# Kernel optimization log

Measured on AMD Instinct MI355X. Metric: run time of the kernel, lower is better.

## Reference

```python
import jax, jax.numpy as jnp
import numpy as np

N = 50000       # nodes
E = 800000      # edges (avg degree 16)
IN = 256        # in_features
HEAD = 4        # attention heads (conv1/conv2 out_channels)
F_OUT = 32      # mlp output features per head


def setup_inputs() -> dict:
    key = jax.random.key(0)
    ks = jax.random.split(key, 6)
    feat = jax.random.normal(ks[0], (N, IN), dtype=jnp.float32)
    edge_index = jax.random.randint(ks[1], (2, E), 0, N, dtype=jnp.int64)
    s = 1.0 / np.sqrt(IN)
    # mlp: Linear(IN -> HEAD*F_OUT)
    W_mlp = jax.random.uniform(ks[2], (IN, HEAD * F_OUT), jnp.float32, -s, s)
    b_mlp = jnp.zeros((HEAD * F_OUT,), jnp.float32)
    # conv1/conv2: 1x1 Conv1d(IN -> HEAD) == linear projection
    W1 = jax.random.uniform(ks[3], (HEAD, IN), jnp.float32, -s, s)
    b1 = jnp.zeros((HEAD,), jnp.float32)
    W2 = jax.random.uniform(ks[4], (HEAD, IN), jnp.float32, -s, s)
    b2 = jnp.zeros((HEAD,), jnp.float32)
    eps = jnp.zeros((1,), jnp.float32)  # trainable eps, init 0
    return {"feat": feat, "edge_index": edge_index, "W_mlp": W_mlp,
            "b_mlp": b_mlp, "W1": W1, "b1": b1, "W2": W2, "b2": b2,
            "eps": eps}


def reference(feat, edge_index, W_mlp, b_mlp, W1, b1, W2, b2, eps):
    n = feat.shape[0]
    head = W1.shape[0]
    # mlp: [N, IN] -> [N, head*F] -> [head, N, F]
    x = (feat @ W_mlp + b_mlp).reshape(n, head, -1).transpose(1, 0, 2)
    # 1x1 conv projections -> per-node attention logits [head, N]
    h1 = (feat @ W1.T + b1).T
    h2 = (feat @ W2.T + b2).T
    src = edge_index[0]  # edge[0]
    dst = edge_index[1]  # edge[1]
    # per-edge attention value, relu (dropout=0 -> identity): [head, E]
    v = jax.nn.relu(h1[:, src] + h2[:, dst])
    # gather neighbor features and weight: [head, E, F]
    msg = x[:, dst, :] * v[:, :, None]
    # scatter-add into destination nodes indexed by src: [N, head, F]
    agg = jax.ops.segment_sum(msg.transpose(1, 0, 2), src, num_segments=n)
    h_prime = agg.transpose(1, 0, 2) + eps[0] * x   # [head, N, F]
    # permute(1,0,2).reshape(N, -1) -> [N, head*F]
    return h_prime.transpose(1, 0, 2).reshape(n, -1)
```

## Files before the change

kernel.cpp:

```cpp
#include <hip/hip_runtime.h>

#define NN   50000
#define EE   800000
#define INF  256
#define COUT 128
#define BTROWS 144
#define PROJ_BLOCKS 782
#define CAP  52

#define NB   196
#define BCAP 4608
#define EPB  2048
#define SC_BLOCKS ((EE + EPB - 1) / EPB)
#define BT_BLOCKS 144

typedef __attribute__((ext_vector_type(8))) short short8;
typedef __attribute__((ext_vector_type(4))) float f32x4;

__device__ __forceinline__ float b2f(unsigned short u) {
    union { unsigned int i; float f; } c;
    c.i = ((unsigned int)u) << 16;
    return c.f;
}
__device__ __forceinline__ unsigned short f2b(float f) {
    union { float f; unsigned int i; } c;
    c.f = f;
    unsigned int i = c.i;
    unsigned int lsb = (i >> 16) & 1u;
    i += 0x7fffu + lsb;
    return (unsigned short)(i >> 16);
}
__device__ __forceinline__ float blo(unsigned int u) {
    union { unsigned int i; float f; } c; c.i = u << 16; return c.f;
}
__device__ __forceinline__ float bhi(unsigned int u) {
    union { unsigned int i; float f; } c; c.i = u & 0xffff0000u; return c.f;
}

__global__ __launch_bounds__(256) void bt_scatter_kernel(
    const float* __restrict__ Wm, const float* __restrict__ W1,
    const float* __restrict__ W2,
    unsigned short* __restrict__ BT,
    const int* __restrict__ edge,
    int* __restrict__ bcnt,
    unsigned int* __restrict__ bedges)
{
    __shared__ int lhist[NB];
    __shared__ int lbase[NB];
    const int t = threadIdx.x;

    if (blockIdx.x < BT_BLOCKS) {
        const int n = blockIdx.x;
        const int k = t;
        float v;
        if      (n < 128) v = Wm[k * COUT + n];
        else if (n < 132) v = W1[(n - 128) * INF + k];
        else if (n < 136) v = W2[(n - 132) * INF + k];
        else              v = 0.f;
        BT[n * INF + k] = f2b(v);
        return;
    }

    if (t < NB) lhist[t] = 0;
    __syncthreads();

    const int e0 = (blockIdx.x - BT_BLOCKS) * EPB;
    int s[8], d[8], pos[8];
    #pragma unroll
    for (int k = 0; k < 8; k++) {
        const int e = e0 + k * 256 + t;
        if (e < EE) {
            s[k] = edge[e];
            d[k] = edge[EE + e];
            pos[k] = atomicAdd(&lhist[s[k] >> 8], 1);
        } else {
            pos[k] = -1;
        }
    }
    __syncthreads();
    if (t < NB) lbase[t] = atomicAdd(&bcnt[t * 16], lhist[t]);
    __syncthreads();
    #pragma unroll
    for (int k = 0; k < 8; k++) {
        if (pos[k] >= 0) {
            const int b = s[k] >> 8;
            const int p = lbase[b] + pos[k];
            if (p < BCAP)
                bedges[b * BCAP + p] =
                    ((unsigned int)(s[k] & 255) << 16) | (unsigned int)d[k];
        }
    }
}

#define LSTRIDE 72
#define SMEM_A_BYTES (64 * LSTRIDE * 2)
#define SMEM_BYTES   (SMEM_A_BYTES + BTROWS * LSTRIDE * 2)
__global__ __launch_bounds__(256) void proj_build_kernel(
    const float* __restrict__ feat,
    const unsigned short* __restrict__ BT,
    const float* __restrict__ bm,
    const float* __restrict__ b1,
    const float* __restrict__ b2,
    unsigned short* __restrict__ x_out,
    unsigned short* __restrict__ hh,
    const unsigned int* __restrict__ bedges,
    const int* __restrict__ bcnt,
    unsigned short* __restrict__ sdst,
    int* __restrict__ cursor)
{
    __shared__ alignas(16) char smem[SMEM_BYTES];
    const int t = threadIdx.x;

    if (blockIdx.x >= PROJ_BLOCKS) {
        unsigned short* ladj = (unsigned short*)smem;
        int* lcur = (int*)(smem + 26624);
        const int b = blockIdx.x - PROJ_BLOCKS;
        lcur[t] = 0;
        __syncthreads();

        const int cnt = min(bcnt[b * 16], BCAP);
        for (int i = t; i < cnt; i += 256) {
            const unsigned int pk = bedges[b * BCAP + i];
            const int n = (int)(pk >> 16);
            const int p = atomicAdd(&lcur[n], 1);
            if (p < CAP) ladj[n * CAP + p] = (unsigned short)(pk & 0xffffu);
        }
        __syncthreads();

        const int node0 = b << 8;
        const int nvalid = min(256, NN - node0);
        const int nu8 = nvalid * (CAP / 4);
        unsigned long long* gs = (unsigned long long*)(sdst + (size_t)node0 * CAP);
        const unsigned long long* ls = (const unsigned long long*)ladj;
        for (int i = t; i < nu8; i += 256) gs[i] = ls[i];
        if (t < nvalid) cursor[node0 + t] = min(lcur[t], CAP);
        return;
    }

    short* lA = (short*)smem;
    short* lB = (short*)(smem + SMEM_A_BYTES);

    const int lane  = t & 63;
    const int wave  = t >> 6;
    const int quad  = lane >> 4;
    const int col   = lane & 15;
    const int node0 = blockIdx.x * 64;

    const int arow = t >> 4;
    const int ac4  = t & 15;

    f32x4 acc[9];
    #pragma unroll
    for (int i = 0; i < 9; i++) acc[i] = (f32x4){0.f, 0.f, 0.f, 0.f};

    float4 fr[4][4];
    #pragma unroll
    for (int kc = 0; kc < 4; kc++) {
        #pragma unroll
        for (int p = 0; p < 4; p++) {
            const int grow = node0 + p * 16 + arow;
            fr[kc][p] = (grow < NN)
                ? *(const float4*)(feat + grow * INF + kc * 64 + ac4 * 4)
                : make_float4(0.f, 0.f, 0.f, 0.f);
        }
    }

    #pragma unroll
    for (int kc = 0; kc < 4; kc++) {
        const int k0 = kc * 64;
        #pragma unroll
        for (int p = 0; p < 4; p++) {
            short4 s;
            s.x = (short)f2b(fr[kc][p].x); s.y = (short)f2b(fr[kc][p].y);
            s.z = (short)f2b(fr[kc][p].z); s.w = (short)f2b(fr[kc][p].w);
            *(short4*)&lA[(p * 16 + arow) * LSTRIDE + ac4 * 4] = s;
        }
        #pragma unroll
        for (int p = 0; p < 5; p++) {
            const int idx = p * 256 + t;
            if (idx < (BTROWS * 64) / 8) {
                const int row = idx >> 3;
                const int c8  = idx & 7;
                uint4 u = *(const uint4*)(BT + row * INF + k0 + c8 * 8);
                *(uint4*)&lB[row * LSTRIDE + c8 * 8] = u;
            }
        }
        __syncthreads();

        #pragma unroll
        for (int ks = 0; ks < 2; ks++) {
            short8 a = *(const short8*)&lA[(wave * 16 + col) * LSTRIDE + ks * 32 + quad * 8];
            #pragma unroll
            for (int nt = 0; nt < 9; nt++) {
                short8 b = *(const short8*)&lB[(nt * 16 + col) * LSTRIDE + ks * 32 + quad * 8];
                acc[nt] = __builtin_amdgcn_mfma_f32_16x16x32_bf16(a, b, acc[nt], 0, 0, 0);
            }
        }
        __syncthreads();
    }

    const int rbase = node0 + wave * 16 + quad * 4;
    #pragma unroll
    for (int nt = 0; nt < 8; nt++) {
        const float bias = bm[nt * 16 + col];
        #pragma unroll
        for (int r = 0; r < 4; r++) {
            const int row = rbase + r;
            if (row < NN) x_out[row * COUT + nt * 16 + col] = f2b(acc[nt][r] + bias);
        }
    }
    if (col < 8) {
        const float bias = (col < 4) ? b1[col] : b2[col - 4];
        #pragma unroll
        for (int r = 0; r < 4; r++) {
            const int row = rbase + r;
            if (row < NN) hh[row * 8 + col] = f2b(acc[8][r] + bias);
        }
    }
}

__global__ __launch_bounds__(256) void accum_kernel(
    const int* __restrict__ cursor,
    const unsigned short* __restrict__ sdst,
    const unsigned short* __restrict__ x,
    const unsigned short* __restrict__ hh,
    const float* __restrict__ eps,
    float* __restrict__ out)
{
    const int lane = threadIdx.x & 63;
    const int node = blockIdx.x * 4 + (threadIdx.x >> 6);
    if (node >= NN) return;

    const int sub = lane & 15;
    const int g   = lane >> 4;
    const int h   = sub >> 2;

    const int deg = min(cursor[node], CAP);

    ushort4 h1u = *(const ushort4*)(hh + node * 8);

    int dv = 0;
    unsigned int vv01 = 0, vv23 = 0;
    if (lane < deg) {
        dv = (int)sdst[node * CAP + lane];
        ushort4 h2u = *(const ushort4*)(hh + dv * 8 + 4);
        const float v0 = b2f(h1u.x) + b2f(h2u.x);
        const float v1 = b2f(h1u.y) + b2f(h2u.y);
        const float v2 = b2f(h1u.z) + b2f(h2u.z);
        const float v3 = b2f(h1u.w) + b2f(h2u.w);
        vv01 = (unsigned int)f2b(v0) | ((unsigned int)f2b(v1) << 16);
        vv23 = (unsigned int)f2b(v2) | ((unsigned int)f2b(v3) << 16);
    }

    float acc[8];
    #pragma unroll
    for (int r = 0; r < 8; r++) acc[r] = 0.f;

    for (int i0 = 0; i0 < deg; i0 += 4) {
        const int idx = i0 + g;
        const int d = __shfl(dv, idx);
        const unsigned int u01 = (unsigned int)__shfl((int)vv01, idx);
        const unsigned int u23 = (unsigned int)__shfl((int)vv23, idx);
        const unsigned int uh = (h & 2) ? u23 : u01;
        const unsigned short vb = (h & 1) ? (unsigned short)(uh >> 16)
                                          : (unsigned short)(uh & 0xffffu);
        const float v = b2f(vb);
        if (idx < deg && v > 0.f) {
            const uint4 u0 = *(const uint4*)(x + d * COUT + sub * 8);
            acc[0] = fmaf(blo(u0.x), v, acc[0]);
            acc[1] = fmaf(bhi(u0.x), v, acc[1]);
            acc[2] = fmaf(blo(u0.y), v, acc[2]);
            acc[3] = fmaf(bhi(u0.y), v, acc[3]);
            acc[4] = fmaf(blo(u0.z), v, acc[4]);
            acc[5] = fmaf(bhi(u0.z), v, acc[5]);
            acc[6] = fmaf(blo(u0.w), v, acc[6]);
            acc[7] = fmaf(bhi(u0.w), v, acc[7]);
        }
    }

    #pragma unroll
    for (int r = 0; r < 8; r++) {
        acc[r] += __shfl_xor(acc[r], 16);
        acc[r] += __shfl_xor(acc[r], 32);
    }

    if (lane < 16) {
        const float e = eps[0];
        const uint4 u0 = *(const uint4*)(x + node * COUT + sub * 8);
        unsigned int uu[4] = {u0.x, u0.y, u0.z, u0.w};
        #pragma unroll
        for (int q = 0; q < 4; q++) {
            acc[2 * q]     = fmaf(e, blo(uu[q]), acc[2 * q]);
            acc[2 * q + 1] = fmaf(e, bhi(uu[q]), acc[2 * q + 1]);
        }
        float* o = out + node * COUT + sub * 8;
        *(float4*)(o)     = make_float4(acc[0], acc[1], acc[2], acc[3]);
        *(float4*)(o + 4) = make_float4(acc[4], acc[5], acc[6], acc[7]);
    }
}

extern "C" void kernel_launch(void* const* d_in, const int* in_sizes, int n_in,
                              void* d_out, int out_size, void* d_ws, size_t ws_size,
                              hipStream_t stream) {
    const float* feat = (const float*)d_in[0];
    const int*   edge = (const int*)d_in[1];
    const float* Wm   = (const float*)d_in[2];
    const float* bm   = (const float*)d_in[3];
    const float* W1   = (const float*)d_in[4];
    const float* b1   = (const float*)d_in[5];
    const float* W2   = (const float*)d_in[6];
    const float* b2   = (const float*)d_in[7];
    const float* eps  = (const float*)d_in[8];

    char* ws = (char*)d_ws;
    unsigned short* x      = (unsigned short*)ws;
    unsigned short* hh     = (unsigned short*)(ws + 12800000);
    int*            cursor = (int*)(ws + 13600000);
    unsigned short* sdst   = (unsigned short*)(ws + 13800000);

    unsigned short* BT     = (unsigned short*)d_out;
    int*            bcnt   = (int*)((char*)d_out + 131072);
    unsigned int*   bedges = (unsigned int*)((char*)d_out + 262144);

    hipMemsetAsync(bcnt, 0, NB * 16 * sizeof(int), stream);
    bt_scatter_kernel<<<BT_BLOCKS + SC_BLOCKS, 256, 0, stream>>>(
        Wm, W1, W2, BT, edge, bcnt, bedges);
    proj_build_kernel<<<PROJ_BLOCKS + NB, 256, 0, stream>>>(
        feat, BT, bm, b1, b2, x, hh, bedges, bcnt, sdst, cursor);
    accum_kernel<<<(NN + 3) / 4, 256, 0, stream>>>(cursor, sdst, x, hh, eps,
                                                   (float*)d_out);
}
```

Measured before the change: 176.3 us.

## Load A fragments directly from global into registers; halve edge bucket size

The projection GEMM no longer stages the feature tile through LDS. Each lane loads its own MFMA A-fragment straight from global memory, converts it to bf16 in registers and prefetches the next k-chunk while the current one runs. Edge bucketing now uses 128-node buckets (391 buckets, smaller capacity), which shrinks the LDS per build block so it fits the reduced shared allocation. The aim is to cut LDS traffic and footprint for higher occupancy, at the cost of less coalesced global reads for A and more bucket atomics.

Result: slower. 182.7 us (+3.6%).

```diff
diff --git a/kernel.cpp b/kernel.cpp
--- a/kernel.cpp
+++ b/kernel.cpp
@@ -8,8 +8,8 @@
 #define PROJ_BLOCKS 782
 #define CAP  52
 
-#define NB   196
-#define BCAP 4608
+#define NB   391
+#define BCAP 2432
 #define EPB  2048
 #define SC_BLOCKS ((EE + EPB - 1) / EPB)
 #define BT_BLOCKS 144
@@ -61,7 +61,7 @@
         return;
     }
 
-    if (t < NB) lhist[t] = 0;
+    for (int i = t; i < NB; i += 256) lhist[i] = 0;
     __syncthreads();
 
     const int e0 = (blockIdx.x - BT_BLOCKS) * EPB;
@@ -72,29 +72,29 @@
         if (e < EE) {
             s[k] = edge[e];
             d[k] = edge[EE + e];
-            pos[k] = atomicAdd(&lhist[s[k] >> 8], 1);
+            pos[k] = atomicAdd(&lhist[s[k] >> 7], 1);
         } else {
             pos[k] = -1;
         }
     }
     __syncthreads();
-    if (t < NB) lbase[t] = atomicAdd(&bcnt[t * 16], lhist[t]);
+    for (int i = t; i < NB; i += 256)
+        lbase[i] = atomicAdd(&bcnt[i * 16], lhist[i]);
     __syncthreads();
     #pragma unroll
     for (int k = 0; k < 8; k++) {
         if (pos[k] >= 0) {
-            const int b = s[k] >> 8;
+            const int b = s[k] >> 7;
             const int p = lbase[b] + pos[k];
             if (p < BCAP)
                 bedges[b * BCAP + p] =
-                    ((unsigned int)(s[k] & 255) << 16) | (unsigned int)d[k];
+                    ((unsigned int)(s[k] & 127) << 16) | (unsigned int)d[k];
         }
     }
 }
 
 #define LSTRIDE 72
-#define SMEM_A_BYTES (64 * LSTRIDE * 2)
-#define SMEM_BYTES   (SMEM_A_BYTES + BTROWS * LSTRIDE * 2)
+#define SMEM_BYTES (BTROWS * LSTRIDE * 2)
 __global__ __launch_bounds__(256) void proj_build_kernel(
     const float* __restrict__ feat,
     const unsigned short* __restrict__ BT,
@@ -113,9 +113,9 @@
 
     if (blockIdx.x >= PROJ_BLOCKS) {
         unsigned short* ladj = (unsigned short*)smem;
-        int* lcur = (int*)(smem + 26624);
+        int* lcur = (int*)(smem + 13312);
         const int b = blockIdx.x - PROJ_BLOCKS;
-        lcur[t] = 0;
+        if (t < 128) lcur[t] = 0;
         __syncthreads();
 
         const int cnt = min(bcnt[b * 16], BCAP);
@@ -127,8 +127,8 @@
         }
         __syncthreads();
 
-        const int node0 = b << 8;
-        const int nvalid = min(256, NN - node0);
+        const int node0 = b << 7;
+        const int nvalid = min(128, NN - node0);
         const int nu8 = nvalid * (CAP / 4);
         unsigned long long* gs = (unsigned long long*)(sdst + (size_t)node0 * CAP);
         const unsigned long long* ls = (const unsigned long long*)ladj;
@@ -137,8 +137,7 @@
         return;
     }
 
-    short* lA = (short*)smem;
-    short* lB = (short*)(smem + SMEM_A_BYTES);
+    short* lB = (short*)smem;
 
     const int lane  = t & 63;
     const int wave  = t >> 6;
@@ -146,35 +145,22 @@
     const int col   = lane & 15;
     const int node0 = blockIdx.x * 64;
 
-    const int arow = t >> 4;
-    const int ac4  = t & 15;
+    const int arow = node0 + wave * 16 + col;
+    const float* aptr = feat + (size_t)(arow < NN ? arow : 0) * INF + quad * 8;
 
     f32x4 acc[9];
     #pragma unroll
     for (int i = 0; i < 9; i++) acc[i] = (f32x4){0.f, 0.f, 0.f, 0.f};
 
-    float4 fr[4][4];
-    #pragma unroll
-    for (int kc = 0; kc < 4; kc++) {
-        #pragma unroll
-        for (int p = 0; p < 4; p++) {
-            const int grow = node0 + p * 16 + arow;
-            fr[kc][p] = (grow < NN)
-                ? *(const float4*)(feat + grow * INF + kc * 64 + ac4 * 4)
-                : make_float4(0.f, 0.f, 0.f, 0.f);
-        }
-    }
+    float4 fa0 = *(const float4*)(aptr);
+    float4 fa1 = *(const float4*)(aptr + 4);
+    float4 fa2 = *(const float4*)(aptr + 32);
+    float4 fa3 = *(const float4*)(aptr + 36);
+    float4 fn0, fn1, fn2, fn3;
 
     #pragma unroll
     for (int kc = 0; kc < 4; kc++) {
         const int k0 = kc * 64;
-        #pragma unroll
-        for (int p = 0; p < 4; p++) {
-            short4 s;
-            s.x = (short)f2b(fr[kc][p].x); s.y = (short)f2b(fr[kc][p].y);
-            s.z = (short)f2b(fr[kc][p].z); s.w = (short)f2b(fr[kc][p].w);
-            *(short4*)&lA[(p * 16 + arow) * LSTRIDE + ac4 * 4] = s;
-        }
         #pragma unroll
         for (int p = 0; p < 5; p++) {
             const int idx = p * 256 + t;
@@ -187,16 +173,37 @@
         }
         __syncthreads();
 
-        #pragma unroll
-        for (int ks = 0; ks < 2; ks++) {
-            short8 a = *(const short8*)&lA[(wave * 16 + col) * LSTRIDE + ks * 32 + quad * 8];
-            #pragma unroll
-            for (int nt = 0; nt < 9; nt++) {
-                short8 b = *(const short8*)&lB[(nt * 16 + col) * LSTRIDE + ks * 32 + quad * 8];
-                acc[nt] = __builtin_amdgcn_mfma_f32_16x16x32_bf16(a, b, acc[nt], 0, 0, 0);
-            }
+        if (kc < 3) {
+            const float* ap = aptr + (kc + 1) * 64;
+            fn0 = *(const float4*)(ap);
+            fn1 = *(const float4*)(ap + 4);
+            fn2 = *(const float4*)(ap + 32);
+            fn3 = *(const float4*)(ap + 36);
+        }
+
+        short8 a0, a1;
+        a0[0] = (short)f2b(fa0.x); a0[1] = (short)f2b(fa0.y);
+        a0[2] = (short)f2b(fa0.z); a0[3] = (short)f2b(fa0.w);
+        a0[4] = (short)f2b(fa1.x); a0[5] = (short)f2b(fa1.y);
+        a0[6] = (short)f2b(fa1.z); a0[7] = (short)f2b(fa1.w);
+        a1[0] = (short)f2b(fa2.x); a1[1] = (short)f2b(fa2.y);
+        a1[2] = (short)f2b(fa2.z); a1[3] = (short)f2b(fa2.w);
+        a1[4] = (short)f2b(fa3.x); a1[5] = (short)f2b(fa3.y);
+        a1[6] = (short)f2b(fa3.z); a1[7] = (short)f2b(fa3.w);
+
+        #pragma unroll
+        for (int nt = 0; nt < 9; nt++) {
+            short8 b0 = *(const short8*)&lB[(nt * 16 + col) * LSTRIDE + quad * 8];
+            acc[nt] = __builtin_amdgcn_mfma_f32_16x16x32_bf16(a0, b0, acc[nt], 0, 0, 0);
+        }
+        #pragma unroll
+        for (int nt = 0; nt < 9; nt++) {
+            short8 b1f = *(const short8*)&lB[(nt * 16 + col) * LSTRIDE + 32 + quad * 8];
+            acc[nt] = __builtin_amdgcn_mfma_f32_16x16x32_bf16(a1, b1f, acc[nt], 0, 0, 0);
         }
         __syncthreads();
+
+        fa0 = fn0; fa1 = fn1; fa2 = fn2; fa3 = fn3;
     }
 
     const int rbase = node0 + wave * 16 + quad * 4;
```
